# Optimization experiments

Measured on AMD Instinct MI355X. Metric: run time of the kernel, lower is better.

## Reference

```python
import jax, jax.numpy as jnp
import numpy as np

IDIM, H, LAYERS = 80, 256, 2
S_TOK, S_DIM, N_HEADS = 5, 128, 4
B, T = 64, 1024


def _gru_layer(x, Wih, Whh, bih, bhh):
    # x: [B,T,in] -> [B,T,H]; PyTorch gate order: reset, update, new
    Bn, Tn, _ = x.shape
    Hn = Whh.shape[1]
    xg = jnp.swapaxes(x @ Wih.T + bih, 0, 1)  # [T,B,3H]

    def step(h, xt):
        gh = h @ Whh.T + bhh
        r = jax.nn.sigmoid(xt[:, :Hn] + gh[:, :Hn])
        z = jax.nn.sigmoid(xt[:, Hn:2 * Hn] + gh[:, Hn:2 * Hn])
        n = jnp.tanh(xt[:, 2 * Hn:] + r * gh[:, 2 * Hn:])
        h = (1.0 - z) * n + z * h
        return h, h

    h0 = jnp.zeros((Bn, Hn), x.dtype)
    _, ys = jax.lax.scan(step, h0, xg)
    return jnp.swapaxes(ys, 0, 1)


def setup_inputs() -> dict:
    key = jax.random.key(0)
    ks = jax.random.split(key, 20)
    s = 0.02
    inp = {
        'feats_averaged': jax.random.normal(ks[0], (B, T, IDIM), jnp.float32),
        'style_tokens': jax.random.normal(ks[1], (1, S_TOK, S_DIM), jnp.float32),
        'Wih0': jax.random.normal(ks[2], (3 * H, IDIM), jnp.float32) * s,
        'Whh0': jax.random.normal(ks[3], (3 * H, H), jnp.float32) * s,
        'bih0': jnp.zeros((3 * H,), jnp.float32),
        'bhh0': jnp.zeros((3 * H,), jnp.float32),
        'Wih1': jax.random.normal(ks[4], (3 * H, H), jnp.float32) * s,
        'Whh1': jax.random.normal(ks[5], (3 * H, H), jnp.float32) * s,
        'bih1': jnp.zeros((3 * H,), jnp.float32),
        'bhh1': jnp.zeros((3 * H,), jnp.float32),
        'q_w': jax.random.normal(ks[6], (H, H), jnp.float32) * s,
        'k_w': jax.random.normal(ks[7], (H, S_DIM), jnp.float32) * s,
        'v_w': jax.random.normal(ks[8], (H, S_DIM), jnp.float32) * s,
        'in_b': jnp.zeros((3 * H,), jnp.float32),
        'out_w': jax.random.normal(ks[9], (H, H), jnp.float32) * s,
        'out_b': jnp.zeros((H,), jnp.float32),
    }
    return inp


def reference(feats_averaged, style_tokens, Wih0, Whh0, bih0, bhh0,
              Wih1, Whh1, bih1, bhh1, q_w, k_w, v_w, in_b, out_w, out_b):
    outs = _gru_layer(feats_averaged, Wih0, Whh0, bih0, bhh0)
    outs = _gru_layer(outs, Wih1, Whh1, bih1, bhh1)  # [B,T,H]

    E = q_w.shape[0]
    hd = E // N_HEADS
    bq, bk, bv = in_b[:E], in_b[E:2 * E], in_b[2 * E:]
    # Per-timestep attention over the same 5 style tokens == one batched attention
    q = (outs @ q_w.T + bq) * (1.0 / jnp.sqrt(jnp.asarray(hd, outs.dtype)))
    k = style_tokens @ k_w.T + bk  # [1,S,E]
    v = style_tokens @ v_w.T + bv
    Bn, Tn, _ = q.shape
    Sn = k.shape[1]
    q = q.reshape(Bn, Tn, N_HEADS, hd)
    k = jnp.broadcast_to(k.reshape(1, Sn, N_HEADS, hd), (Bn, Sn, N_HEADS, hd))
    v = jnp.broadcast_to(v.reshape(1, Sn, N_HEADS, hd), (Bn, Sn, N_HEADS, hd))
    scores = jnp.einsum('bthd,bshd->bhts', q, k)  # [B,Hh,T,S]
    attn = jax.nn.softmax(scores, axis=-1)
    ctx = jnp.einsum('bhts,bshd->bthd', attn, v).reshape(Bn, Tn, E)
    return ctx @ out_w.T + out_b
```

## Files before the change

### kernel.cpp

```cpp
#include <hip/hip_runtime.h>
#include <hip/hip_bf16.h>
#include <cmath>

typedef unsigned int u32;
typedef unsigned short u16;
typedef _Float16 f16;
typedef f16 h2 __attribute__((ext_vector_type(2)));
typedef f16 h8 __attribute__((ext_vector_type(8)));
typedef float f32x4 __attribute__((ext_vector_type(4)));
typedef u16 u16x4 __attribute__((ext_vector_type(4)));

#define Bn 64
#define Tn 1024
#define IDIM 80
#define Hn 256
#define G3 768
#define STOK 5
#define SDIM 128
#define MROWS (Bn*Tn)
#define CH 8

__device__ __forceinline__ u16 f2h(float f) {
  union { f16 h; u16 u; } c; c.h = (f16)f; return c.u;
}
__device__ __forceinline__ float h2f(u16 u) {
  union { f16 h; u16 u2; } c; c.u2 = u; return (float)c.h;
}
__device__ __forceinline__ float frcp(float x) {
#if __has_builtin(__builtin_amdgcn_rcpf)
  return __builtin_amdgcn_rcpf(x);
#else
  return 1.f / x;
#endif
}
__device__ __forceinline__ float fsig(float x) { return frcp(1.f + __expf(-x)); }
__device__ __forceinline__ float ftanh(float x) { return 1.f - 2.f * frcp(1.f + __expf(2.f * x)); }
__device__ __forceinline__ int sdot4(u32 a, u32 b, int c) {
#if __has_builtin(__builtin_amdgcn_sdot4)
  return __builtin_amdgcn_sdot4(a, b, c, false);
#else
  int r = c;
#pragma unroll
  for (int j = 0; j < 4; ++j)
    r += (int)(char)(a >> (8 * j)) * (int)(char)(b >> (8 * j));
  return r;
#endif
}
__device__ __forceinline__ int qsumi(int v) {
  v += __builtin_amdgcn_mov_dpp(v, 0xB1, 0xF, 0xF, true);
  v += __builtin_amdgcn_mov_dpp(v, 0x4E, 0xF, 0xF, true);
  return v;
}

__device__ __forceinline__ void lds_barrier() {
  asm volatile("s_waitcnt lgkmcnt(0)" ::: "memory");
  __builtin_amdgcn_sched_barrier(0);
  __builtin_amdgcn_s_barrier();
  __builtin_amdgcn_sched_barrier(0);
}

__global__ void k_cvt_f16(const float* __restrict__ in, u16* __restrict__ out, int n) {
  int i = blockIdx.x * blockDim.x + threadIdx.x;
  int st = gridDim.x * blockDim.x;
  for (; i < n; i += st) out[i] = f2h(in[i]);
}

__global__ void k_wmax(const float* __restrict__ W, float* __restrict__ wmax,
                       float* __restrict__ wsc) {
  int j = blockIdx.x * 256 + threadIdx.x;
  if (j >= G3) return;
  float m = 0.f;
  for (int k = 0; k < Hn; ++k) m = fmaxf(m, fabsf(W[j * Hn + k]));
  wmax[j] = m;
  wsc[j] = m * (1.f / 16129.f);
}

__global__ void k_prep_i8(const float* __restrict__ W, const float* __restrict__ wmax,
                          u32* __restrict__ out) {
  int idx = blockIdx.x * 256 + threadIdx.x;
  if (idx >= G3 * 64) return;
  int tau = idx >> 6, rest = idx & 63;
  int s = rest >> 4, i4p = rest & 15;
  int r = 4 * (tau >> 2) + s;
  int c0 = 64 * (tau & 3) + i4p * 4;
  float m = wmax[r];
  float inv = (m > 0.f) ? (127.f / m) : 0.f;
  u32 pk = 0;
#pragma unroll
  for (int j = 0; j < 4; ++j) {
    int q = (int)lrintf(W[r * Hn + c0 + j] * inv);
    q = (q > 127) ? 127 : (q < -127) ? -127 : q;
    pk |= ((u32)(unsigned char)(char)q) << (8 * j);
  }
  out[idx] = pk;
}

__global__ __launch_bounds__(256) void k_kv(const float* __restrict__ st,
                                            const float* __restrict__ kw,
                                            const float* __restrict__ vw,
                                            const float* __restrict__ inb,
                                            float* __restrict__ kv) {
  int e = threadIdx.x;
  for (int s = 0; s < STOK; ++s) {
    float ak = inb[Hn + e], av = inb[2 * Hn + e];
    for (int d = 0; d < SDIM; ++d) {
      float x = st[s * SDIM + d];
      ak += x * kw[e * SDIM + d];
      av += x * vw[e * SDIM + d];
    }
    kv[s * Hn + e] = ak;
    kv[STOK * Hn + s * Hn + e] = av;
  }
}

template <int MODE>
__global__ __launch_bounds__(256) void k_gemm_bt(const u16* __restrict__ A,
                                                 const u16* __restrict__ B,
                                                 const float* __restrict__ bias,
                                                 float scale, void* __restrict__ Cout,
                                                 int M, int N, int K) {
  constexpr int BM = 128, BN = 128, BK = 32, LDT = 40;
  __shared__ __align__(16) u16 As[BM * LDT];
  __shared__ __align__(16) u16 Bs[BN * LDT];
  const int tid = threadIdx.x;
  const int bm0 = blockIdx.x * BM;
  const int bn0 = blockIdx.y * BN;
  const int lane = tid & 63;
  const int wave = tid >> 6;
  const int wm = (wave & 1) * 64;
  const int wn = (wave >> 1) * 64;
  const int lr = lane & 15;
  const int kg = lane >> 4;
  const int srow = tid >> 1, sch = tid & 1;

  f32x4 acc[4][4] = {};

  for (int k0 = 0; k0 < K; k0 += BK) {
    {
      const u16* gp = A + (size_t)(bm0 + srow) * K + k0 + sch * 16;
      u16* lp = &As[srow * LDT + sch * 16];
      if (k0 + BK <= K) {
        *(uint4*)lp = *(const uint4*)gp;
        *(uint4*)(lp + 8) = *(const uint4*)(gp + 8);
      } else {
        for (int i = 0; i < 16; ++i) {
          int k = k0 + sch * 16 + i;
          lp[i] = (k < K) ? gp[i] : (u16)0;
        }
      }
    }
    {
      const u16* gp = B + (size_t)(bn0 + srow) * K + k0 + sch * 16;
      u16* lp = &Bs[srow * LDT + sch * 16];
      if (k0 + BK <= K) {
        *(uint4*)lp = *(const uint4*)gp;
        *(uint4*)(lp + 8) = *(const uint4*)(gp + 8);
      } else {
        for (int i = 0; i < 16; ++i) {
          int k = k0 + sch * 16 + i;
          lp[i] = (k < K) ? gp[i] : (u16)0;
        }
      }
    }
    __syncthreads();

    h8 af[4], bfr[4];
#pragma unroll
    for (int mi = 0; mi < 4; ++mi)
      af[mi] = *(const h8*)&As[(wm + mi * 16 + lr) * LDT + kg * 8];
#pragma unroll
    for (int ni = 0; ni < 4; ++ni)
      bfr[ni] = *(const h8*)&Bs[(wn + ni * 16 + lr) * LDT + kg * 8];
#pragma unroll
    for (int mi = 0; mi < 4; ++mi)
#pragma unroll
      for (int ni = 0; ni < 4; ++ni)
        acc[mi][ni] = __builtin_amdgcn_mfma_f32_16x16x32_f16(af[mi], bfr[ni], acc[mi][ni], 0, 0, 0);
    __syncthreads();
  }

#pragma unroll
  for (int mi = 0; mi < 4; ++mi)
#pragma unroll
    for (int ni = 0; ni < 4; ++ni) {
      int m0 = bm0 + wm + mi * 16 + kg * 4;
      int col = bn0 + wn + ni * 16 + lr;
      float bv = bias ? bias[col] : 0.f;
      if (MODE == 2) {
        int bidx = m0 >> 10, t0 = m0 & 1023;
        u16x4 pk;
#pragma unroll
        for (int r = 0; r < 4; ++r) pk[r] = f2h((acc[mi][ni][r] + bv) * scale);
        *(u16x4*)((u16*)Cout + (size_t)bidx * N * Tn + (size_t)col * Tn + t0) = pk;
      } else {
#pragma unroll
        for (int r = 0; r < 4; ++r) {
          float v = (acc[mi][ni][r] + bv) * scale;
          if (MODE == 1)
            ((u16*)Cout)[(size_t)(m0 + r) * N + col] = f2h(v);
          else
            ((float*)Cout)[(size_t)(m0 + r) * N + col] = v;
        }
      }
    }
}

__global__ void __launch_bounds__(768)
__attribute__((amdgpu_waves_per_eu(3, 3)))
k_mega(const u32* __restrict__ Wp8, const float* __restrict__ wscGh,
       const float* __restrict__ bhh,
       u16* __restrict__ xgT, u16* __restrict__ o, float* __restrict__ hst,
       int gruH,
       const u16* __restrict__ gA, const u16* __restrict__ gB,
       const float* __restrict__ gBias, float gScale,
       u16* __restrict__ gC, int gmMode, int gmH, int gmN) {
  const int ngru = (gruH >= 0) ? 64 : 0;
  const int tid = threadIdx.x;
  __shared__ __align__(16) char ldsu[20992];

  if ((int)blockIdx.x < ngru) {
    char* hsh8 = ldsu;
    float* ght = (float*)(ldsu + 256);
    u16* xst = (u16*)(ldsu + 256 + 3072);
    const int b = blockIdx.x;
    const int j = tid & 255;

    u32 wv8[64];
    {
      const uint4* wp = (const uint4*)(Wp8 + (size_t)tid * 64);
#pragma unroll
      for (int i = 0; i < 16; ++i) ((uint4*)wv8)[i] = wp[i];
    }
#pragma unroll
    for (int i = 0; i < 64; ++i) asm volatile("" : "+v"(wv8[i]));
    const float wsc = wscGh[tid];

    float b0 = bhh[j], b1 = bhh[j + Hn], b2 = bhh[j + 2 * Hn];
    float hreg = (gruH > 0) ? hst[b * Hn + j] : 0.f;
    if (tid < Hn) hsh8[tid] = (char)(int)lrintf(hreg * 127.f);

    const u16* xrow = xgT + (size_t)b * G3 * Tn + (size_t)tid * Tn;
    u16* ob = o + (size_t)b * Tn * Hn;
    const uint4* hq4 = (const uint4*)(hsh8 + (tid & 3) * 64);
    const int tc0 = gruH * 64, tc1 = tc0 + 64;

    uint4 xchunk = *(const uint4*)(xrow + tc0 * CH);
    __syncthreads();

    for (int tc = tc0; tc < tc1; ++tc) {
#pragma unroll
      for (int u = 0; u < CH; ++u) {
        u32 w = ((u32*)&xchunk)[u >> 1];
        u16 piece = (u & 1) ? (u16)(w >> 16) : (u16)w;
        xst[u * G3 + tid] = piece;
      }
      int tcn = (tc + 1 < Tn / CH) ? tc + 1 : tc;
      xchunk = *(const uint4*)(xrow + tcn * CH);

#pragma unroll
      for (int u = 0; u < CH; ++u) {
        int A0 = 0, A1 = 0, A2 = 0, A3 = 0;
#pragma unroll
        for (int i = 0; i < 4; ++i) {
          uint4 hv = hq4[i];
#pragma unroll
          for (int p = 0; p < 4; ++p) {
            u32 hw = (&hv.x)[p];
            A0 = sdot4(wv8[i * 4 + p], hw, A0);
            A1 = sdot4(wv8[16 + i * 4 + p], hw, A1);
            A2 = sdot4(wv8[32 + i * 4 + p], hw, A2);
            A3 = sdot4(wv8[48 + i * 4 + p], hw, A3);
          }
        }
        A0 = qsumi(A0); A1 = qsumi(A1); A2 = qsumi(A2); A3 = qsumi(A3);
        int q = tid & 3;
        int isel = (q == 0) ? A0 : (q == 1) ? A1 : (q == 2) ? A2 : A3;
        ght[tid] = (float)isel * wsc;
        lds_barrier();
        {
          float gr = ght[j] + b0;
          float gz = ght[j + Hn] + b1;
          float gn = ght[j + 2 * Hn] + b2;
          float xr = h2f(xst[u * G3 + j]);
          float xz = h2f(xst[u * G3 + j + Hn]);
          float xn = h2f(xst[u * G3 + j + 2 * Hn]);
          float r = fsig(xr + gr);
          float z = fsig(xz + gz);
          float n = ftanh(xn + r * gn);
          hreg = (1.f - z) * n + z * hreg;
          if (tid < Hn) {
            ob[(size_t)(tc * CH + u) * Hn + tid] = f2h(hreg);
            hsh8[tid] = (char)(int)lrintf(hreg * 127.f);
          }
        }
        lds_barrier();
      }
    }
    if (tid < Hn) hst[b * Hn + tid] = hreg;
    return;
  }

  if (gmMode == 0) return;
  constexpr int LDT = 40;
  u16* As = (u16*)ldsu;
  u16* Bs = (u16*)(ldsu + 10240);
  const int idx = blockIdx.x - ngru;
  const int mt = idx & 255, nt = idx >> 8;
  const int bm0 = (mt >> 2) * Tn + gmH * 512 + (mt & 3) * 128;
  const int bn0 = nt * 128;
  const int lane = tid & 63;
  const int wave = tid >> 6;
  const int wm = (wave & 1) * 64;
  const int wn = (wave >> 1) * 64;
  const int lr = lane & 15;
  const int kg = lane >> 4;
  const int srow = (tid & 255) >> 1, sch = tid & 1;

  f32x4 acc[4][4] = {};

  for (int k0 = 0; k0 < 256; k0 += 32) {
    if (tid < 256) {
      const u16* gp = gA + (size_t)(bm0 + srow) * 256 + k0 + sch * 16;
      u16* lp = &As[srow * LDT + sch * 16];
      *(uint4*)lp = *(const uint4*)gp;
      *(uint4*)(lp + 8) = *(const uint4*)(gp + 8);
      const u16* gp2 = gB + (size_t)(bn0 + srow) * 256 + k0 + sch * 16;
      u16* lp2 = &Bs[srow * LDT + sch * 16];
      *(uint4*)lp2 = *(const uint4*)gp2;
      *(uint4*)(lp2 + 8) = *(const uint4*)(gp2 + 8);
    }
    __syncthreads();
    if (tid < 256) {
      h8 af[4], bfr[4];
#pragma unroll
      for (int mi = 0; mi < 4; ++mi)
        af[mi] = *(const h8*)&As[(wm + mi * 16 + lr) * LDT + kg * 8];
#pragma unroll
      for (int ni = 0; ni < 4; ++ni)
        bfr[ni] = *(const h8*)&Bs[(wn + ni * 16 + lr) * LDT + kg * 8];
#pragma unroll
      for (int mi = 0; mi < 4; ++mi)
#pragma unroll
        for (int ni = 0; ni < 4; ++ni)
          acc[mi][ni] = __builtin_amdgcn_mfma_f32_16x16x32_f16(af[mi], bfr[ni], acc[mi][ni], 0, 0, 0);
    }
    __syncthreads();
  }

  if (tid < 256) {
#pragma unroll
    for (int mi = 0; mi < 4; ++mi)
#pragma unroll
      for (int ni = 0; ni < 4; ++ni) {
        int m0 = bm0 + wm + mi * 16 + kg * 4;
        int col = bn0 + wn + ni * 16 + lr;
        float bv = gBias[col];
        if (gmMode == 2) {
          int bidx = m0 >> 10, t0 = m0 & 1023;
          u16x4 pk;
#pragma unroll
          for (int r = 0; r < 4; ++r) pk[r] = f2h((acc[mi][ni][r] + bv) * gScale);
          *(u16x4*)(gC + (size_t)bidx * gmN * Tn + (size_t)col * Tn + t0) = pk;
        } else {
#pragma unroll
          for (int r = 0; r < 4; ++r)
            gC[(size_t)(m0 + r) * gmN + col] = f2h((acc[mi][ni][r] + bv) * gScale);
        }
      }
  }
}

__global__ __launch_bounds__(256) void k_attn(const u16* __restrict__ q,
                                              const float* __restrict__ kv,
                                              u16* __restrict__ ctx) {
  __shared__ float ks[STOK * Hn], vs[STOK * Hn];
  int tid = threadIdx.x;
  for (int i = tid; i < STOK * Hn; i += 256) {
    ks[i] = kv[i];
    vs[i] = kv[STOK * Hn + i];
  }
  __syncthreads();
  size_t row = (size_t)blockIdx.x * 256 + tid;
  const u16* qr = q + row * Hn;
  u16* cr = ctx + row * Hn;
#pragma unroll
  for (int h = 0; h < 4; ++h) {
    float sc[STOK] = {0.f, 0.f, 0.f, 0.f, 0.f};
    for (int d = 0; d < 64; ++d) {
      float qv = h2f(qr[h * 64 + d]);
#pragma unroll
      for (int s = 0; s < STOK; ++s) sc[s] += qv * ks[s * Hn + h * 64 + d];
    }
    float m = sc[0];
#pragma unroll
    for (int s = 1; s < STOK; ++s) m = fmaxf(m, sc[s]);
    float p[STOK], sum = 0.f;
#pragma unroll
    for (int s = 0; s < STOK; ++s) { p[s] = __expf(sc[s] - m); sum += p[s]; }
    float inv = 1.f / sum;
    for (int e = 0; e < 64; ++e) {
      float c = 0.f;
#pragma unroll
      for (int s = 0; s < STOK; ++s) c += p[s] * vs[s * Hn + h * 64 + e];
      cr[h * 64 + e] = f2h(c * inv);
    }
  }
}

#define WS_XGT  ((size_t)0)
#define WS_O    ((size_t)100663296)
#define WS_QB   ((size_t)134217728)
#define WS_FB   ((size_t)167772160)
#define WS_W0   ((size_t)178257920)
#define WS_W1   ((size_t)178380800)
#define WS_QW   ((size_t)178774016)
#define WS_OW   ((size_t)178905088)
#define WS_H0P  ((size_t)179036160)
#define WS_H1P  ((size_t)179232768)
#define WS_SC0  ((size_t)179429376)
#define WS_SC1  ((size_t)179432448)
#define WS_MX0  ((size_t)179435520)
#define WS_MX1  ((size_t)179438592)
#define WS_KV   ((size_t)179822592)
#define WS_HST  WS_FB
#define WS_CTX  WS_XGT

extern "C" void kernel_launch(void* const* d_in, const int* in_sizes, int n_in,
                              void* d_out, int out_size, void* d_ws, size_t ws_size,
                              hipStream_t stream) {
  const float* feats = (const float*)d_in[0];
  const float* style = (const float*)d_in[1];
  const float* Wih0 = (const float*)d_in[2];
  const float* Whh0 = (const float*)d_in[3];
  const float* bih0 = (const float*)d_in[4];
  const float* bhh0 = (const float*)d_in[5];
  const float* Wih1 = (const float*)d_in[6];
  const float* Whh1 = (const float*)d_in[7];
  const float* bih1 = (const float*)d_in[8];
  const float* bhh1 = (const float*)d_in[9];
  const float* q_w = (const float*)d_in[10];
  const float* k_w = (const float*)d_in[11];
  const float* v_w = (const float*)d_in[12];
  const float* in_b = (const float*)d_in[13];
  const float* out_w = (const float*)d_in[14];
  const float* out_b = (const float*)d_in[15];

  char* ws = (char*)d_ws;
  u16* xgT = (u16*)(ws + WS_XGT);
  u16* o = (u16*)(ws + WS_O);
  u16* qb = (u16*)(ws + WS_QB);
  u16* fb = (u16*)(ws + WS_FB);
  u16* w0 = (u16*)(ws + WS_W0);
  u16* w1 = (u16*)(ws + WS_W1);
  u16* qw = (u16*)(ws + WS_QW);
  u16* ow = (u16*)(ws + WS_OW);
  u32* h0p = (u32*)(ws + WS_H0P);
  u32* h1p = (u32*)(ws + WS_H1P);
  float* sc0 = (float*)(ws + WS_SC0);
  float* sc1 = (float*)(ws + WS_SC1);
  float* mx0 = (float*)(ws + WS_MX0);
  float* mx1 = (float*)(ws + WS_MX1);
  float* kv = (float*)(ws + WS_KV);
  float* hst = (float*)(ws + WS_HST);
  u16* ctx = (u16*)(ws + WS_CTX);

  auto cvgrid = [](int n) { int g = (n + 255) / 256; return g > 2048 ? 2048 : g; };

  k_cvt_f16<<<cvgrid(MROWS * IDIM), 256, 0, stream>>>(feats, fb, MROWS * IDIM);
  k_cvt_f16<<<cvgrid(G3 * IDIM), 256, 0, stream>>>(Wih0, w0, G3 * IDIM);
  k_cvt_f16<<<cvgrid(G3 * Hn), 256, 0, stream>>>(Wih1, w1, G3 * Hn);
  k_cvt_f16<<<cvgrid(Hn * Hn), 256, 0, stream>>>(q_w, qw, Hn * Hn);
  k_cvt_f16<<<cvgrid(Hn * Hn), 256, 0, stream>>>(out_w, ow, Hn * Hn);
  k_wmax<<<3, 256, 0, stream>>>(Whh0, mx0, sc0);
  k_wmax<<<3, 256, 0, stream>>>(Whh1, mx1, sc1);
  k_prep_i8<<<(G3 * 64 + 255) / 256, 256, 0, stream>>>(Whh0, mx0, h0p);
  k_prep_i8<<<(G3 * 64 + 255) / 256, 256, 0, stream>>>(Whh1, mx1, h1p);
  k_kv<<<1, 256, 0, stream>>>(style, k_w, v_w, in_b, kv);

  dim3 g768(MROWS / 128, G3 / 128);
  k_gemm_bt<2><<<g768, 256, 0, stream>>>(fb, w0, bih0, 1.f, xgT, MROWS, G3, IDIM);

  k_mega<<<64, 768, 0, stream>>>(h0p, sc0, bhh0, xgT, o, hst, 0,
                                 nullptr, nullptr, nullptr, 0.f, nullptr, 0, 0, 0);
  k_mega<<<64 + 1536, 768, 0, stream>>>(h0p, sc0, bhh0, xgT, o, hst, 1,
                                        o, w1, bih1, 1.f, xgT, 2, 0, G3);
  k_mega<<<64 + 1536, 768, 0, stream>>>(h1p, sc1, bhh1, xgT, o, hst, 0,
                                        o, w1, bih1, 1.f, xgT, 2, 1, G3);
  k_mega<<<64 + 512, 768, 0, stream>>>(h1p, sc1, bhh1, xgT, o, hst, 1,
                                       o, qw, in_b, 0.125f, qb, 1, 0, Hn);
  k_mega<<<512, 768, 0, stream>>>(h0p, sc0, bhh0, xgT, o, hst, -1,
                                  o, qw, in_b, 0.125f, qb, 1, 1, Hn);

  k_attn<<<MROWS / 256, 256, 0, stream>>>(qb, kv, ctx);
  dim3 g256t(MROWS / 128, Hn / 128);
  k_gemm_bt<0><<<g256t, 256, 0, stream>>>(ctx, ow, out_b, 1.f, d_out, MROWS, Hn, Hn);
}
```

Baseline: 1.948 ms.

## Remap GRU recurrence so each quad owns one hidden unit, double-buffer h

Reorganizes the recurrent step so that each group of four threads computes all three gates (r, z, n) for one hidden unit. The gate values stay in registers after the quad reduction, which removes the LDS gate staging buffer and one of the two barriers per timestep. The quantized hidden state is double-buffered in LDS so the next step's h can be written without waiting on readers. The block grows from 768 to 1024 threads with 48 packed weights per thread, and the weight packing kernel is changed to match. The GEMM side of the mega-kernel now also runs with 1024-thread blocks under a 4-waves-per-EU bound, which may change its register budget and occupancy.

```diff
diff --git a/kernel.cpp b/kernel.cpp
--- a/kernel.cpp
+++ b/kernel.cpp
@@ -78,19 +78,20 @@
 __global__ void k_prep_i8(const float* __restrict__ W, const float* __restrict__ wmax,
                           u32* __restrict__ out) {
   int idx = blockIdx.x * 256 + threadIdx.x;
-  if (idx >= G3 * 64) return;
-  int tau = idx >> 6, rest = idx & 63;
+  if (idx >= 1024 * 48) return;
+  int tau = idx / 48, rest = idx % 48;
   int s = rest >> 4, i4p = rest & 15;
-  int r = 4 * (tau >> 2) + s;
-  int c0 = 64 * (tau & 3) + i4p * 4;
+  int j = tau >> 2, q = tau & 3;
+  int r = j + 256 * s;
+  int c0 = q * 64 + i4p * 4;
   float m = wmax[r];
   float inv = (m > 0.f) ? (127.f / m) : 0.f;
   u32 pk = 0;
 #pragma unroll
-  for (int j = 0; j < 4; ++j) {
-    int q = (int)lrintf(W[r * Hn + c0 + j] * inv);
-    q = (q > 127) ? 127 : (q < -127) ? -127 : q;
-    pk |= ((u32)(unsigned char)(char)q) << (8 * j);
+  for (int jj = 0; jj < 4; ++jj) {
+    int qv = (int)lrintf(W[r * Hn + c0 + jj] * inv);
+    qv = (qv > 127) ? 127 : (qv < -127) ? -127 : qv;
+    pk |= ((u32)(unsigned char)(char)qv) << (8 * jj);
   }
   out[idx] = pk;
 }
@@ -205,8 +206,8 @@
     }
 }
 
-__global__ void __launch_bounds__(768)
-__attribute__((amdgpu_waves_per_eu(3, 3)))
+__global__ void __launch_bounds__(1024)
+__attribute__((amdgpu_waves_per_eu(4, 4)))
 k_mega(const u32* __restrict__ Wp8, const float* __restrict__ wscGh,
        const float* __restrict__ bhh,
        u16* __restrict__ xgT, u16* __restrict__ o, float* __restrict__ hst,
@@ -220,46 +221,52 @@
 
   if ((int)blockIdx.x < ngru) {
     char* hsh8 = ldsu;
-    float* ght = (float*)(ldsu + 256);
-    u16* xst = (u16*)(ldsu + 256 + 3072);
+    u16* xst = (u16*)(ldsu + 512);
     const int b = blockIdx.x;
-    const int j = tid & 255;
-
-    u32 wv8[64];
+    const int j = tid >> 2;
+    const int q = tid & 3;
+    const int qlead = (q == 0);
+
+    u32 wv8[48];
     {
-      const uint4* wp = (const uint4*)(Wp8 + (size_t)tid * 64);
-#pragma unroll
-      for (int i = 0; i < 16; ++i) ((uint4*)wv8)[i] = wp[i];
-    }
-#pragma unroll
-    for (int i = 0; i < 64; ++i) asm volatile("" : "+v"(wv8[i]));
-    const float wsc = wscGh[tid];
-
-    float b0 = bhh[j], b1 = bhh[j + Hn], b2 = bhh[j + 2 * Hn];
+      const uint4* wp = (const uint4*)(Wp8 + (size_t)tid * 48);
+#pragma unroll
+      for (int i = 0; i < 12; ++i) ((uint4*)wv8)[i] = wp[i];
+    }
+#pragma unroll
+    for (int i = 0; i < 48; ++i) asm volatile("" : "+v"(wv8[i]));
+
+    const float wsc0 = wscGh[j], wsc1 = wscGh[j + Hn], wsc2 = wscGh[j + 2 * Hn];
+    const float b0 = bhh[j], b1 = bhh[j + Hn], b2 = bhh[j + 2 * Hn];
     float hreg = (gruH > 0) ? hst[b * Hn + j] : 0.f;
-    if (tid < Hn) hsh8[tid] = (char)(int)lrintf(hreg * 127.f);
-
-    const u16* xrow = xgT + (size_t)b * G3 * Tn + (size_t)tid * Tn;
+    if (qlead) hsh8[j] = (char)(int)lrintf(hreg * 127.f);
+
+    const u16* xrow = (tid < G3) ? xgT + (size_t)b * G3 * Tn + (size_t)tid * Tn : nullptr;
     u16* ob = o + (size_t)b * Tn * Hn;
-    const uint4* hq4 = (const uint4*)(hsh8 + (tid & 3) * 64);
     const int tc0 = gruH * 64, tc1 = tc0 + 64;
 
-    uint4 xchunk = *(const uint4*)(xrow + tc0 * CH);
+    uint4 xchunk = {};
+    if (tid < G3) xchunk = *(const uint4*)(xrow + tc0 * CH);
+    int rp = 0;
     __syncthreads();
 
     for (int tc = tc0; tc < tc1; ++tc) {
+      if (tid < G3) {
+#pragma unroll
+        for (int u = 0; u < CH; ++u) {
+          u32 w = ((u32*)&xchunk)[u >> 1];
+          u16 piece = (u & 1) ? (u16)(w >> 16) : (u16)w;
+          xst[u * G3 + tid] = piece;
+        }
+        int tcn = (tc + 1 < Tn / CH) ? tc + 1 : tc;
+        xchunk = *(const uint4*)(xrow + tcn * CH);
+      }
+      lds_barrier();
+
 #pragma unroll
       for (int u = 0; u < CH; ++u) {
-        u32 w = ((u32*)&xchunk)[u >> 1];
-        u16 piece = (u & 1) ? (u16)(w >> 16) : (u16)w;
-        xst[u * G3 + tid] = piece;
-      }
-      int tcn = (tc + 1 < Tn / CH) ? tc + 1 : tc;
-      xchunk = *(const uint4*)(xrow + tcn * CH);
-
-#pragma unroll
-      for (int u = 0; u < CH; ++u) {
-        int A0 = 0, A1 = 0, A2 = 0, A3 = 0;
+        const uint4* hq4 = (const uint4*)(hsh8 + rp * 256 + q * 64);
+        int A0 = 0, A1 = 0, A2 = 0;
 #pragma unroll
         for (int i = 0; i < 4; ++i) {
           uint4 hv = hq4[i];
@@ -269,34 +276,28 @@
             A0 = sdot4(wv8[i * 4 + p], hw, A0);
             A1 = sdot4(wv8[16 + i * 4 + p], hw, A1);
             A2 = sdot4(wv8[32 + i * 4 + p], hw, A2);
-            A3 = sdot4(wv8[48 + i * 4 + p], hw, A3);
           }
         }
-        A0 = qsumi(A0); A1 = qsumi(A1); A2 = qsumi(A2); A3 = qsumi(A3);
-        int q = tid & 3;
-        int isel = (q == 0) ? A0 : (q == 1) ? A1 : (q == 2) ? A2 : A3;
-        ght[tid] = (float)isel * wsc;
+        A0 = qsumi(A0); A1 = qsumi(A1); A2 = qsumi(A2);
+        float gr = (float)A0 * wsc0 + b0;
+        float gz = (float)A1 * wsc1 + b1;
+        float gn = (float)A2 * wsc2 + b2;
+        float xr = h2f(xst[u * G3 + j]);
+        float xz = h2f(xst[u * G3 + j + Hn]);
+        float xn = h2f(xst[u * G3 + j + 2 * Hn]);
+        float r = fsig(xr + gr);
+        float z = fsig(xz + gz);
+        float n = ftanh(xn + r * gn);
+        hreg = (1.f - z) * n + z * hreg;
+        if (qlead) {
+          ob[(size_t)(tc * CH + u) * Hn + j] = f2h(hreg);
+          hsh8[(rp ^ 1) * 256 + j] = (char)(int)lrintf(hreg * 127.f);
+        }
         lds_barrier();
-        {
-          float gr = ght[j] + b0;
-          float gz = ght[j + Hn] + b1;
-          float gn = ght[j + 2 * Hn] + b2;
-          float xr = h2f(xst[u * G3 + j]);
-          float xz = h2f(xst[u * G3 + j + Hn]);
-          float xn = h2f(xst[u * G3 + j + 2 * Hn]);
-          float r = fsig(xr + gr);
-          float z = fsig(xz + gz);
-          float n = ftanh(xn + r * gn);
-          hreg = (1.f - z) * n + z * hreg;
-          if (tid < Hn) {
-            ob[(size_t)(tc * CH + u) * Hn + tid] = f2h(hreg);
-            hsh8[tid] = (char)(int)lrintf(hreg * 127.f);
-          }
-        }
-        lds_barrier();
-      }
-    }
-    if (tid < Hn) hst[b * Hn + tid] = hreg;
+        rp ^= 1;
+      }
+    }
+    if (qlead) hst[b * Hn + j] = hreg;
     return;
   }
 
@@ -473,23 +474,23 @@
   k_cvt_f16<<<cvgrid(Hn * Hn), 256, 0, stream>>>(out_w, ow, Hn * Hn);
   k_wmax<<<3, 256, 0, stream>>>(Whh0, mx0, sc0);
   k_wmax<<<3, 256, 0, stream>>>(Whh1, mx1, sc1);
-  k_prep_i8<<<(G3 * 64 + 255) / 256, 256, 0, stream>>>(Whh0, mx0, h0p);
-  k_prep_i8<<<(G3 * 64 + 255) / 256, 256, 0, stream>>>(Whh1, mx1, h1p);
+  k_prep_i8<<<(1024 * 48 + 255) / 256, 256, 0, stream>>>(Whh0, mx0, h0p);
+  k_prep_i8<<<(1024 * 48 + 255) / 256, 256, 0, stream>>>(Whh1, mx1, h1p);
   k_kv<<<1, 256, 0, stream>>>(style, k_w, v_w, in_b, kv);
 
   dim3 g768(MROWS / 128, G3 / 128);
   k_gemm_bt<2><<<g768, 256, 0, stream>>>(fb, w0, bih0, 1.f, xgT, MROWS, G3, IDIM);
 
-  k_mega<<<64, 768, 0, stream>>>(h0p, sc0, bhh0, xgT, o, hst, 0,
-                                 nullptr, nullptr, nullptr, 0.f, nullptr, 0, 0, 0);
-  k_mega<<<64 + 1536, 768, 0, stream>>>(h0p, sc0, bhh0, xgT, o, hst, 1,
-                                        o, w1, bih1, 1.f, xgT, 2, 0, G3);
-  k_mega<<<64 + 1536, 768, 0, stream>>>(h1p, sc1, bhh1, xgT, o, hst, 0,
-                                        o, w1, bih1, 1.f, xgT, 2, 1, G3);
-  k_mega<<<64 + 512, 768, 0, stream>>>(h1p, sc1, bhh1, xgT, o, hst, 1,
-                                       o, qw, in_b, 0.125f, qb, 1, 0, Hn);
-  k_mega<<<512, 768, 0, stream>>>(h0p, sc0, bhh0, xgT, o, hst, -1,
-                                  o, qw, in_b, 0.125f, qb, 1, 1, Hn);
+  k_mega<<<64, 1024, 0, stream>>>(h0p, sc0, bhh0, xgT, o, hst, 0,
+                                  nullptr, nullptr, nullptr, 0.f, nullptr, 0, 0, 0);
+  k_mega<<<64 + 1536, 1024, 0, stream>>>(h0p, sc0, bhh0, xgT, o, hst, 1,
+                                         o, w1, bih1, 1.f, xgT, 2, 0, G3);
+  k_mega<<<64 + 1536, 1024, 0, stream>>>(h1p, sc1, bhh1, xgT, o, hst, 0,
+                                         o, w1, bih1, 1.f, xgT, 2, 1, G3);
+  k_mega<<<64 + 512, 1024, 0, stream>>>(h1p, sc1, bhh1, xgT, o, hst, 1,
+                                        o, qw, in_b, 0.125f, qb, 1, 0, Hn);
+  k_mega<<<512, 1024, 0, stream>>>(h0p, sc0, bhh0, xgT, o, hst, -1,
+                                   o, qw, in_b, 0.125f, qb, 1, 1, Hn);
 
   k_attn<<<MROWS / 256, 256, 0, stream>>>(qb, kv, ctx);
   dim3 g256t(MROWS / 128, Hn / 128);
```

Measured after the change: 2.024 ms. +3.9%, slower.
